# Performance work log

Hardware: AMD Instinct MI355X
Metric: run time of the kernel (lower is better)

Reference implementation:

```python
import jax, jax.numpy as jnp
import numpy as np

B, C, W, H, N = 8, 128, 48, 48, 8192


def setup_inputs() -> dict:
    key = jax.random.key(0)
    ks = jax.random.split(key, 16)
    s = 1.0 / np.sqrt(C)
    inp = {
        "feat0": jax.random.normal(ks[0], (B, C, W, H), jnp.float32),
        "feat1": jax.random.normal(ks[1], (B, C, N), jnp.float32),
        "geo_embed": jax.random.normal(ks[2], (B, W * H, C), jnp.float32),
        # Linear weights stored as [in, out]; biases [out].
        "Wq": jax.random.normal(ks[3], (C, C), jnp.float32) * s,
        "bq": jnp.zeros((C,), jnp.float32),
        "Wk": jax.random.normal(ks[4], (C, C), jnp.float32) * s,
        "bk": jnp.zeros((C,), jnp.float32),
        "Wv": jax.random.normal(ks[5], (C, C), jnp.float32) * s,
        "bv": jnp.zeros((C,), jnp.float32),
        "Wo": jax.random.normal(ks[6], (C, C), jnp.float32) * s,
        "bo": jnp.zeros((C,), jnp.float32),
        "Wg": jax.random.normal(ks[7], (C, C), jnp.float32) * s,
        "bg": jnp.zeros((C,), jnp.float32),
        "Wgate": jax.random.normal(ks[8], (2 * C, 1), jnp.float32) * (1.0 / np.sqrt(2 * C)),
        "bgate": jnp.zeros((1,), jnp.float32),
    }
    return inp


def reference(feat0, feat1, geo_embed, Wq, bq, Wk, bk, Wv, bv, Wo, bo, Wg, bg, Wgate, bgate):
    b, c, w, h = feat0.shape
    # b c w h -> b (w h) c
    q_in = feat0.reshape(b, c, w * h).transpose(0, 2, 1)
    pq = q_in @ Wq + bq  # [b, wh, c]

    geo = geo_embed @ Wg + bg  # [b, wh, c]
    gate = jax.nn.sigmoid(jnp.concatenate([pq, geo], axis=-1) @ Wgate + bgate)  # [b, wh, 1]
    pq = pq + gate * geo

    kv_in = feat1.transpose(0, 2, 1)  # [b, n, c]
    pk = kv_in @ Wk + bk
    pv = kv_in @ Wv + bv

    energy = jnp.einsum('bqc,bnc->bqn', pq, pk)  # [b, wh, n]
    # NOTE: original scales AFTER softmax (non-standard, faithful):
    attention = jax.nn.softmax(energy, axis=-1) / jnp.sqrt(jnp.asarray(c, energy.dtype))
    out = jnp.einsum('bqn,bnc->bqc', attention, pv) @ Wo + bo  # [b, wh, c]
    out = out.transpose(0, 2, 1).reshape(b, c, w, h)

    geo_r = geo.transpose(0, 2, 1).reshape(b, c, w, h)
    out = out * (1.0 + jax.nn.sigmoid(geo_r))
    out = out + feat0
    return out
```

## Files before the change

kernel.cpp:

```cpp
#include <hip/hip_runtime.h>

#define B_ 8
#define C_ 128
#define WH_ 2304
#define N_ 8192

typedef unsigned short u16;
typedef float f32x4 __attribute__((ext_vector_type(4)));
typedef short s16x8 __attribute__((ext_vector_type(8)));
typedef short s16x4 __attribute__((ext_vector_type(4)));
typedef unsigned int u32x2 __attribute__((ext_vector_type(2)));

typedef const unsigned int __attribute__((address_space(1))) ga_u32;
typedef unsigned int __attribute__((address_space(3))) lds_u32;

#define LOG2E 1.4426950408889634f
#define MOFF  64.0f

__device__ __forceinline__ float bf2f(u16 u){
    union { unsigned int i; float f; } x; x.i = ((unsigned int)u) << 16; return x.f;
}
__device__ __forceinline__ u16 f2bf(float f){
    union { float f; unsigned int i; } x; x.f = f;
    unsigned int r = x.i + 0x7fffu + ((x.i >> 16) & 1u);
    return (u16)(r >> 16);
}
__device__ __forceinline__ int swz(int row, int col){
    return row*128 + ((((col >> 3) ^ (row & 15)) << 3) | (col & 7));
}
__device__ __forceinline__ f32x4 fzero(){ f32x4 z = {0.f, 0.f, 0.f, 0.f}; return z; }
__device__ __forceinline__ f32x4 fmoff(){ f32x4 z = {-MOFF, -MOFF, -MOFF, -MOFF}; return z; }
__device__ __forceinline__ f32x4 mfma16(s16x8 a, s16x8 b, f32x4 c){
    return __builtin_amdgcn_mfma_f32_16x16x32_bf16(a, b, c, 0, 0, 0);
}
__device__ __forceinline__ void gld16(const void* g, void* l){
    __builtin_amdgcn_global_load_lds((ga_u32*)g, (lds_u32*)l, 16, 0, 0);
}
__device__ __forceinline__ s16x8 ldsf(const u16* p){ return *(const s16x8*)p; }
__device__ __forceinline__ s16x8 cvt8(const float* p){
    s16x8 r;
    #pragma unroll
    for (int j = 0; j < 8; j++) r[j] = (short)f2bf(p[j]);
    return r;
}

__global__ __launch_bounds__(256) void k_prep(
    const float* __restrict__ Wq, const float* __restrict__ Wk,
    const float* __restrict__ Wv, const float* __restrict__ Wo,
    const float* __restrict__ Wg, u16* __restrict__ Wt)
{
    const int gid = blockIdx.x*256 + threadIdx.x;
    const int mi = gid >> 14, e = gid & 16383;
    const int o = e >> 7, i = e & 127;
    const float* src = (mi==0)?Wq:(mi==1)?Wk:(mi==2)?Wv:(mi==3)?Wo:Wg;
    Wt[mi*16384 + o*128 + i] = f2bf(src[i*128 + o]);
}

__device__ __forceinline__ void proj_kv_body(
    char* smem, int blk,
    const float* __restrict__ feat1,
    const float* __restrict__ bk, const float* __restrict__ bv,
    const u16* __restrict__ Wt,
    u16* __restrict__ Kb, u16* __restrict__ Vb)
{
    u16* Af = (u16*)smem;
    const int t = threadIdx.x;
    const int b = blk >> 5;
    const int n0 = (blk & 31) * 256;
    for (int idx = t; idx < 8192; idx += 512){
        const int nl = (idx & 63) << 2, c = idx >> 6;
        const f32x4 v = *(const f32x4*)&feat1[((size_t)b*C_ + c)*N_ + n0 + nl];
        Af[swz(nl+0, c)] = f2bf(v[0]); Af[swz(nl+1, c)] = f2bf(v[1]);
        Af[swz(nl+2, c)] = f2bf(v[2]); Af[swz(nl+3, c)] = f2bf(v[3]);
    }
    __syncthreads();
    const int lane = t & 63, w = t >> 6, qq = lane >> 4, m = lane & 15;
    s16x8 aA[2][4];
    #pragma unroll
    for (int rt = 0; rt < 2; rt++){
        const int ar = w*32 + rt*16 + m;
        #pragma unroll
        for (int kt = 0; kt < 4; kt++)
            aA[rt][kt] = ldsf(&Af[ar*128 + (((kt*4 + qq) ^ (ar & 15)) << 3)]);
    }
    const u16* WkT = Wt + 16384;
    const u16* WvT = Wt + 32768;
    f32x4 acc[2][8];
    #pragma unroll
    for (int rt = 0; rt < 2; rt++){
        #pragma unroll
        for (int ct = 0; ct < 8; ct++) acc[rt][ct] = fzero();
    }
    #pragma unroll
    for (int kt = 0; kt < 4; kt++){
        #pragma unroll
        for (int ct = 0; ct < 8; ct++){
            const int bn = ct*16 + m;
            const s16x8 bf = *(const s16x8*)&WkT[bn*128 + kt*32 + qq*8];
            acc[0][ct] = mfma16(aA[0][kt], bf, acc[0][ct]);
            acc[1][ct] = mfma16(aA[1][kt], bf, acc[1][ct]);
        }
    }
    u16* Ko = (u16*)smem;
    #pragma unroll
    for (int ct = 0; ct < 8; ct++){
        const int col = ct*16 + m;
        const float bkv = bk[col];
        #pragma unroll
        for (int rt = 0; rt < 2; rt++){
            #pragma unroll
            for (int i = 0; i < 4; i++)
                Ko[swz(w*32 + rt*16 + qq*4 + i, col)] = f2bf(acc[rt][ct][i] + bkv);
        }
    }
    #pragma unroll
    for (int j = 0; j < 8; j++){
        const int chunk = j*64 + lane;
        const int row = w*32 + (chunk >> 4);
        const int cb = chunk & 15;
        s16x8 v = ldsf(&Ko[row*128 + ((cb ^ (row & 15)) << 3)]);
        *(s16x8*)&Kb[((size_t)b*N_ + n0 + row)*C_ + cb*8] = v;
    }
    #pragma unroll
    for (int rt = 0; rt < 2; rt++){
        #pragma unroll
        for (int ct = 0; ct < 8; ct++) acc[rt][ct] = fzero();
    }
    #pragma unroll
    for (int kt = 0; kt < 4; kt++){
        #pragma unroll
        for (int ct = 0; ct < 8; ct++){
            const int bn = ct*16 + m;
            const s16x8 bf = *(const s16x8*)&WvT[bn*128 + kt*32 + qq*8];
            acc[0][ct] = mfma16(aA[0][kt], bf, acc[0][ct]);
            acc[1][ct] = mfma16(aA[1][kt], bf, acc[1][ct]);
        }
    }
    __syncthreads();
    u16* Tv = (u16*)smem;
    #pragma unroll
    for (int ct = 0; ct < 8; ct++){
        const int col = ct*16 + m;
        const float bvv = bv[col];
        #pragma unroll
        for (int rt = 0; rt < 2; rt++){
            #pragma unroll
            for (int i = 0; i < 4; i++)
                Tv[col*258 + w*32 + rt*16 + qq*4 + i] = f2bf(acc[rt][ct][i] + bvv);
        }
    }
    __syncthreads();
    for (int idx = t; idx < 16384; idx += 512){
        const int c = idx >> 7, nl = (idx & 127) << 1;
        const unsigned int v = *(const unsigned int*)&Tv[c*258 + nl];
        *(unsigned int*)&Vb[((size_t)b*C_ + c)*N_ + n0 + nl] = v;
    }
}

__device__ __forceinline__ void proj_qg_body(
    char* smem, int blk,
    const float* __restrict__ feat0, const float* __restrict__ geo,
    const float* __restrict__ bq, const float* __restrict__ bg,
    const float* __restrict__ Wgate, const float* __restrict__ bgate,
    const u16* __restrict__ Wt,
    u16* __restrict__ Qb, u16* __restrict__ Gb)
{
    u16* Aq = (u16*)smem;
    const int t = threadIdx.x;
    const int b = blk / 18;
    const int r0 = (blk % 18) * 128;
    for (int idx = t; idx < 4096; idx += 512){
        const int r = (idx & 31) << 2, c = idx >> 5;
        const f32x4 v = *(const f32x4*)&feat0[((size_t)b*C_ + c)*WH_ + r0 + r];
        Aq[swz(r+0, c)] = f2bf(v[0]); Aq[swz(r+1, c)] = f2bf(v[1]);
        Aq[swz(r+2, c)] = f2bf(v[2]); Aq[swz(r+3, c)] = f2bf(v[3]);
    }
    __syncthreads();
    const int lane = t & 63, w = t >> 6, qq = lane >> 4, m = lane & 15;
    const int ar = w*16 + m;
    s16x8 aQ[4], aG[4];
    #pragma unroll
    for (int kt = 0; kt < 4; kt++){
        aQ[kt] = ldsf(&Aq[ar*128 + (((kt*4 + qq) ^ (ar & 15)) << 3)]);
        aG[kt] = cvt8(&geo[((size_t)b*WH_ + r0 + ar)*C_ + kt*32 + qq*8]);
    }
    f32x4 accq[8], accg[8];
    #pragma unroll
    for (int ct = 0; ct < 8; ct++){ accq[ct] = fzero(); accg[ct] = fzero(); }
    #pragma unroll
    for (int kt = 0; kt < 4; kt++){
        #pragma unroll
        for (int ct = 0; ct < 8; ct++){
            const int bn = ct*16 + m;
            const s16x8 b1 = *(const s16x8*)&Wt[bn*128 + kt*32 + qq*8];
            const s16x8 b2 = *(const s16x8*)&Wt[65536 + bn*128 + kt*32 + qq*8];
            accq[ct] = mfma16(aQ[kt], b1, accq[ct]);
            accg[ct] = mfma16(aG[kt], b2, accg[ct]);
        }
    }
    float bqv[8], bgv[8], w1v[8], w2v[8];
    #pragma unroll
    for (int ct = 0; ct < 8; ct++){
        int col = ct*16 + m;
        bqv[ct] = bq[col]; bgv[ct] = bg[col];
        w1v[ct] = Wgate[col]; w2v[ct] = Wgate[C_ + col];
    }
    const float bg0 = bgate[0];
    float gate[4];
    #pragma unroll
    for (int i = 0; i < 4; i++){
        float p = 0.f;
        #pragma unroll
        for (int ct = 0; ct < 8; ct++)
            p += (accq[ct][i] + bqv[ct]) * w1v[ct] + (accg[ct][i] + bgv[ct]) * w2v[ct];
        #pragma unroll
        for (int off = 1; off < 16; off <<= 1) p += __shfl_xor(p, off, 64);
        gate[i] = 1.f / (1.f + __expf(-(p + bg0)));
    }
    u16* St = Aq;
    #pragma unroll
    for (int ct = 0; ct < 8; ct++){
        #pragma unroll
        for (int i = 0; i < 4; i++){
            const float ge = accg[ct][i] + bgv[ct];
            const float pq = accq[ct][i] + bqv[ct] + gate[i] * ge;
            St[swz(w*16 + qq*4 + i, ct*16 + m)] = f2bf(pq * LOG2E);
        }
    }
    #pragma unroll
    for (int j = 0; j < 4; j++){
        const int chunk = j*64 + lane;
        const int row = w*16 + (chunk >> 4);
        const int cb = chunk & 15;
        s16x8 v = ldsf(&St[row*128 + ((cb ^ (row & 15)) << 3)]);
        *(s16x8*)&Qb[((size_t)b*WH_ + r0 + row)*C_ + cb*8] = v;
    }
    #pragma unroll
    for (int ct = 0; ct < 8; ct++){
        #pragma unroll
        for (int i = 0; i < 4; i++)
            St[swz(w*16 + qq*4 + i, ct*16 + m)] = f2bf(accg[ct][i] + bgv[ct]);
    }
    #pragma unroll
    for (int j = 0; j < 4; j++){
        const int chunk = j*64 + lane;
        const int row = w*16 + (chunk >> 4);
        const int cb = chunk & 15;
        s16x8 v = ldsf(&St[row*128 + ((cb ^ (row & 15)) << 3)]);
        *(s16x8*)&Gb[((size_t)b*WH_ + r0 + row)*C_ + cb*8] = v;
    }
}

__global__ __launch_bounds__(512, 4) void k_proj(
    const float* __restrict__ feat1,
    const float* __restrict__ bk, const float* __restrict__ bv,
    const float* __restrict__ feat0, const float* __restrict__ geo,
    const float* __restrict__ bq, const float* __restrict__ bg,
    const float* __restrict__ Wgate, const float* __restrict__ bgate,
    const u16* __restrict__ Wt,
    u16* __restrict__ Kb, u16* __restrict__ Vb,
    u16* __restrict__ Qb, u16* __restrict__ Gb)
{
    __shared__ __attribute__((aligned(16))) char smem[66048];
    if (blockIdx.x < 256)
        proj_kv_body(smem, blockIdx.x, feat1, bk, bv, Wt, Kb, Vb);
    else
        proj_qg_body(smem, blockIdx.x - 256, feat0, geo, bq, bg, Wgate, bgate, Wt, Qb, Gb);
}

__global__ __launch_bounds__(1024, 4) void k_flash(
    const u16* __restrict__ Qb, const u16* __restrict__ Kb, const u16* __restrict__ Vb,
    u16* __restrict__ Opart, float* __restrict__ Lp)
{
    __shared__ __attribute__((aligned(16))) u16 KP0[128*128];
    __shared__ __attribute__((aligned(16))) u16 KP1[128*128];
    __shared__ __attribute__((aligned(16))) u16 Vt0[128*128];
    __shared__ __attribute__((aligned(16))) u16 Vt1[128*128];
    const int t = threadIdx.x;
    const int lane = t & 63, w = t >> 6;
    const int q = lane >> 4, m = lane & 15;
    const int b = blockIdx.x & 7;
    const int s = blockIdx.x >> 3;

    f32x4 o[8];
    float lr;
    s16x8 qf[4];

    auto issue = [&](int k){
        const int u = s*18 + k;
        const int n0 = (u & 63) * 128;
        u16* KPd = (k & 1) ? KP1 : KP0;
        u16* Vtd = (k & 1) ? Vt1 : Vt0;
        #pragma unroll
        for (int j = 0; j < 2; j++){
            const int r = w*8 + j*4 + q;
            const int pr = (r & 96) | ((r & 12) << 1) | ((r & 16) >> 2) | (r & 3);
            gld16(Kb + ((size_t)b*N_ + n0 + pr)*C_ + ((m ^ (r & 15)) << 3), &KPd[(w*8 + j*4)*128]);
            gld16(Vb + ((size_t)b*C_ + r)*N_ + n0 + ((m ^ (r & 15)) << 3), &Vtd[(w*8 + j*4)*128]);
        }
    };
    auto load_q = [&](int qb){
        const size_t qrow0 = (size_t)b*WH_ + qb*256;
        #pragma unroll
        for (int kt = 0; kt < 4; kt++)
            qf[kt] = *(const s16x8*)&Qb[(qrow0 + w*16 + m)*C_ + kt*32 + q*8];
    };
    auto zero_acc = [&](){
        #pragma unroll
        for (int ct = 0; ct < 8; ct++) o[ct] = fzero();
        lr = 0.f;
    };
    auto flush = [&](int qb){
        const int sf = (qb * 64) / 18;
        const size_t pbase = ((size_t)(b*9 + qb)*5 + (s - sf)) * 256;
        #pragma unroll
        for (int ct = 0; ct < 8; ct++){
            u32x2 pk;
            pk.x = (unsigned int)f2bf(o[ct][0]) | ((unsigned int)f2bf(o[ct][1]) << 16);
            pk.y = (unsigned int)f2bf(o[ct][2]) | ((unsigned int)f2bf(o[ct][3]) << 16);
            *(u32x2*)&Opart[(pbase + w*16 + m)*128 + ct*16 + q*4] = pk;
        }
        float l0 = lr;
        l0 += __shfl_xor(l0, 16, 64); l0 += __shfl_xor(l0, 32, 64);
        if (q == 0) Lp[pbase + w*16 + m] = l0;
    };

    issue(0);
    int cur_qb = (s*18) >> 6;
    load_q(cur_qb);
    zero_acc();

    for (int k = 0; k < 18; k++){
        __syncthreads();
        if (k < 17) issue(k + 1);
        const u16* KPc = (k & 1) ? KP1 : KP0;
        const u16* Vtc = (k & 1) ? Vt1 : Vt0;

        #pragma unroll
        for (int h = 0; h < 2; h++){
            s16x4 pexp[4];
            #pragma unroll
            for (int n2 = 0; n2 < 4; n2++){
                const int nt = h*4 + n2;
                f32x4 s0 = fmoff();
                const int bn = nt*16 + m;
                #pragma unroll
                for (int kt = 0; kt < 4; kt++){
                    s16x8 kf = ldsf(&KPc[bn*128 + (((kt*4 + q) ^ (bn & 15)) << 3)]);
                    s0 = mfma16(kf, qf[kt], s0);
                }
                #pragma unroll
                for (int i = 0; i < 4; i++){
                    float e0 = exp2f(s0[i]);
                    lr += e0;
                    pexp[n2][i] = (short)f2bf(e0);
                }
            }
            const s16x8 p80 = __builtin_shufflevector(pexp[0], pexp[1], 0,1,2,3,4,5,6,7);
            const s16x8 p81 = __builtin_shufflevector(pexp[2], pexp[3], 0,1,2,3,4,5,6,7);
            #pragma unroll
            for (int ct = 0; ct < 8; ct++){
                const int cc = ct*16 + m;
                const int pair0 = h*2;
                s16x8 vf0 = ldsf(&Vtc[cc*128 + ((((pair0+0)*4 + q) ^ (cc & 15)) << 3)]);
                s16x8 vf1 = ldsf(&Vtc[cc*128 + ((((pair0+1)*4 + q) ^ (cc & 15)) << 3)]);
                o[ct] = mfma16(vf0, p80, o[ct]);
                o[ct] = mfma16(vf1, p81, o[ct]);
            }
        }
        const int nqb = (k < 17) ? ((s*18 + k + 1) >> 6) : -1;
        if (nqb != cur_qb){
            flush(cur_qb);
            if (nqb >= 0){ load_q(nqb); zero_acc(); cur_qb = nqb; }
        }
    }
}

__global__ __launch_bounds__(256) void k_out(
    const u16* __restrict__ Opart, const float* __restrict__ Lp,
    const float* __restrict__ bo, const u16* __restrict__ Wt,
    const u16* __restrict__ Gb, const float* __restrict__ feat0,
    float* __restrict__ outp)
{
    __shared__ __attribute__((aligned(16))) u16 AO[128*128];
    __shared__ u16 Tr[128*130];
    const int t = threadIdx.x;
    const int bqt = blockIdx.x;
    const int qt2 = bqt >> 1, half = bqt & 1;
    const int b = qt2 / 9, qb = qt2 % 9;
    const int gr0 = qb*256 + half*128;
    const u16* WoT = Wt + 49152;
    const float rsC = 0.088388347648318447f;
    const int sf = (qb*64) / 18;
    const int sl = (qb*64 + 63) / 18;
    const int cnt = sl - sf + 1;
    for (int idx = t; idx < 128*16; idx += 256){
        int r = idx >> 4, cb = idx & 15;
        float num[8];
        #pragma unroll
        for (int j = 0; j < 8; j++) num[j] = 0.f;
        float den = 0.f;
        for (int ss = 0; ss < cnt; ss++){
            const size_t base = ((size_t)qt2*5 + ss)*256 + half*128 + r;
            s16x8 v = *(const s16x8*)&Opart[base*128 + cb*8];
            #pragma unroll
            for (int j = 0; j < 8; j++) num[j] += bf2f((u16)v[j]);
            den += Lp[base];
        }
        const float sc = rsC / den;
        s16x8 o8;
        #pragma unroll
        for (int j = 0; j < 8; j++) o8[j] = (short)f2bf(num[j] * sc);
        *(s16x8*)&AO[r*128 + ((cb ^ (r & 15)) << 3)] = o8;
    }
    __syncthreads();
    const int lane = t & 63, w = t >> 6;
    const int q = lane >> 4, m = lane & 15;
    const int rw = w * 32;
    f32x4 acc[2][8];
    #pragma unroll
    for (int rt = 0; rt < 2; rt++){
        #pragma unroll
        for (int ct = 0; ct < 8; ct++) acc[rt][ct] = fzero();
    }
    #pragma unroll
    for (int kt = 0; kt < 4; kt++){
        s16x8 a0, a1;
        { const int ar = rw + m;      a0 = ldsf(&AO[ar*128 + (((kt*4 + q) ^ (ar & 15)) << 3)]); }
        { const int ar = rw + 16 + m; a1 = ldsf(&AO[ar*128 + (((kt*4 + q) ^ (ar & 15)) << 3)]); }
        #pragma unroll
        for (int ct = 0; ct < 8; ct++){
            const s16x8 bb = *(const s16x8*)&WoT[(ct*16 + m)*128 + kt*32 + q*8];
            acc[0][ct] = mfma16(a0, bb, acc[0][ct]);
            acc[1][ct] = mfma16(a1, bb, acc[1][ct]);
        }
    }
    #pragma unroll
    for (int ct = 0; ct < 8; ct++){
        const int col = ct*16 + m;
        const float bov = bo[col];
        #pragma unroll
        for (int rt = 0; rt < 2; rt++){
            #pragma unroll
            for (int i = 0; i < 4; i++){
                const int rl = rw + rt*16 + q*4 + i;
                const float gv = bf2f(Gb[((size_t)b*WH_ + gr0 + rl)*C_ + col]);
                const float sg = 1.f / (1.f + __expf(-gv));
                Tr[rl*130 + col] = f2bf((acc[rt][ct][i] + bov) * (1.f + sg));
            }
        }
    }
    __syncthreads();
    for (int idx = t; idx < 128*128; idx += 256){
        int c = idx >> 7, wh = idx & 127;
        float v = bf2f(Tr[wh*130 + c]) + feat0[(size_t)(b*C_ + c)*WH_ + gr0 + wh];
        outp[(size_t)(b*C_ + c)*WH_ + gr0 + wh] = v;
    }
}

extern "C" void kernel_launch(void* const* d_in, const int* in_sizes, int n_in,
                              void* d_out, int out_size, void* d_ws, size_t ws_size,
                              hipStream_t stream)
{
    (void)in_sizes; (void)n_in; (void)out_size; (void)ws_size;
    const float* feat0 = (const float*)d_in[0];
    const float* feat1 = (const float*)d_in[1];
    const float* geo   = (const float*)d_in[2];
    const float* Wq = (const float*)d_in[3];  const float* bq = (const float*)d_in[4];
    const float* Wk = (const float*)d_in[5];  const float* bk = (const float*)d_in[6];
    const float* Wv = (const float*)d_in[7];  const float* bv = (const float*)d_in[8];
    const float* Wo = (const float*)d_in[9];  const float* bo = (const float*)d_in[10];
    const float* Wg = (const float*)d_in[11]; const float* bg = (const float*)d_in[12];
    const float* Wgate = (const float*)d_in[13]; const float* bgate = (const float*)d_in[14];
    float* outp = (float*)d_out;
    char* ws = (char*)d_ws;
    size_t off = 0;
    auto alloc = [&](size_t bytes) -> void* {
        void* p = (void*)(ws + off);
        off += (bytes + 255) & ~(size_t)255;
        return p;
    };
    u16* Qb = (u16*)alloc((size_t)B_*WH_*C_*2);
    u16* Gb = (u16*)alloc((size_t)B_*WH_*C_*2);
    u16* Kb = (u16*)alloc((size_t)B_*N_*C_*2);
    u16* Vb = (u16*)alloc((size_t)B_*N_*C_*2);
    u16* Opart = (u16*)alloc((size_t)72*5*256*128*2);
    float* Lp  = (float*)alloc((size_t)72*5*256*4);
    u16* Wt = (u16*)alloc((size_t)5*16384*2);

    k_prep <<<dim3(320), dim3(256), 0, stream>>>(Wq, Wk, Wv, Wo, Wg, Wt);
    k_proj <<<dim3(400), dim3(512), 0, stream>>>(feat1, bk, bv, feat0, geo, bq, bg,
                                                 Wgate, bgate, Wt, Kb, Vb, Qb, Gb);
    k_flash<<<dim3(256), dim3(1024), 0, stream>>>(Qb, Kb, Vb, Opart, Lp);
    k_out  <<<dim3(144), dim3(256), 0, stream>>>(Opart, Lp, bo, Wt, Gb, feat0, outp);
}
```

Measured before the change: 303.4 us.

## Split projection kernel, use packed bf16 converts and MFMA row-sum in flash loop

The merged projection kernel is split into separate K/V and Q/G kernels with smaller tiles and more blocks. The K/V kernel writes V directly from registers instead of staging it through LDS. The flash attention loop now converts exponentials with the hardware packed bf16 instruction and computes the softmax denominator with an MFMA against a ones vector, which removes scalar adds and cross-lane shuffles. This adds one kernel launch, and the row sum is now taken over bf16-rounded probabilities, which is consistent with what feeds the PV MFMA.

Result: faster. 286.1 us (-5.7%).

```diff
diff --git a/kernel.cpp b/kernel.cpp
--- a/kernel.cpp
+++ b/kernel.cpp
@@ -25,6 +25,11 @@
     unsigned int r = x.i + 0x7fffu + ((x.i >> 16) & 1u);
     return (u16)(r >> 16);
 }
+__device__ __forceinline__ unsigned int cvtpk(float a, float b){
+    unsigned int r;
+    asm("v_cvt_pk_bf16_f32 %0, %1, %2" : "=v"(r) : "v"(a), "v"(b));
+    return r;
+}
 __device__ __forceinline__ int swz(int row, int col){
     return row*128 + ((((col >> 3) ^ (row & 15)) << 3) | (col & 7));
 }
@@ -56,121 +61,93 @@
     Wt[mi*16384 + o*128 + i] = f2bf(src[i*128 + o]);
 }
 
-__device__ __forceinline__ void proj_kv_body(
-    char* smem, int blk,
+__global__ __launch_bounds__(512, 4) void k_proj_kv(
     const float* __restrict__ feat1,
     const float* __restrict__ bk, const float* __restrict__ bv,
     const u16* __restrict__ Wt,
     u16* __restrict__ Kb, u16* __restrict__ Vb)
 {
-    u16* Af = (u16*)smem;
+    __shared__ __attribute__((aligned(16))) u16 Af[128*128];
     const int t = threadIdx.x;
-    const int b = blk >> 5;
-    const int n0 = (blk & 31) * 256;
-    for (int idx = t; idx < 8192; idx += 512){
-        const int nl = (idx & 63) << 2, c = idx >> 6;
+    const int b = blockIdx.x >> 6;
+    const int n0 = (blockIdx.x & 63) * 128;
+    for (int idx = t; idx < 128*32; idx += 512){
+        const int nl = (idx & 31) << 2, c = idx >> 5;
         const f32x4 v = *(const f32x4*)&feat1[((size_t)b*C_ + c)*N_ + n0 + nl];
         Af[swz(nl+0, c)] = f2bf(v[0]); Af[swz(nl+1, c)] = f2bf(v[1]);
         Af[swz(nl+2, c)] = f2bf(v[2]); Af[swz(nl+3, c)] = f2bf(v[3]);
     }
     __syncthreads();
     const int lane = t & 63, w = t >> 6, qq = lane >> 4, m = lane & 15;
-    s16x8 aA[2][4];
-    #pragma unroll
-    for (int rt = 0; rt < 2; rt++){
-        const int ar = w*32 + rt*16 + m;
-        #pragma unroll
-        for (int kt = 0; kt < 4; kt++)
-            aA[rt][kt] = ldsf(&Af[ar*128 + (((kt*4 + qq) ^ (ar & 15)) << 3)]);
-    }
+    const int ar = w*16 + m;
+    s16x8 aA[4];
+    #pragma unroll
+    for (int kt = 0; kt < 4; kt++)
+        aA[kt] = ldsf(&Af[ar*128 + (((kt*4 + qq) ^ (ar & 15)) << 3)]);
     const u16* WkT = Wt + 16384;
     const u16* WvT = Wt + 32768;
-    f32x4 acc[2][8];
-    #pragma unroll
-    for (int rt = 0; rt < 2; rt++){
-        #pragma unroll
-        for (int ct = 0; ct < 8; ct++) acc[rt][ct] = fzero();
-    }
+    f32x4 acc[8];
+    #pragma unroll
+    for (int ct = 0; ct < 8; ct++) acc[ct] = fzero();
     #pragma unroll
     for (int kt = 0; kt < 4; kt++){
         #pragma unroll
         for (int ct = 0; ct < 8; ct++){
-            const int bn = ct*16 + m;
-            const s16x8 bf = *(const s16x8*)&WkT[bn*128 + kt*32 + qq*8];
-            acc[0][ct] = mfma16(aA[0][kt], bf, acc[0][ct]);
-            acc[1][ct] = mfma16(aA[1][kt], bf, acc[1][ct]);
-        }
-    }
-    u16* Ko = (u16*)smem;
+            const s16x8 bf = *(const s16x8*)&WkT[(ct*16 + m)*128 + kt*32 + qq*8];
+            acc[ct] = mfma16(aA[kt], bf, acc[ct]);
+        }
+    }
+    u16* Ko = Af;
     #pragma unroll
     for (int ct = 0; ct < 8; ct++){
         const int col = ct*16 + m;
         const float bkv = bk[col];
         #pragma unroll
-        for (int rt = 0; rt < 2; rt++){
-            #pragma unroll
-            for (int i = 0; i < 4; i++)
-                Ko[swz(w*32 + rt*16 + qq*4 + i, col)] = f2bf(acc[rt][ct][i] + bkv);
-        }
-    }
-    #pragma unroll
-    for (int j = 0; j < 8; j++){
+        for (int i = 0; i < 4; i++)
+            Ko[swz(w*16 + qq*4 + i, col)] = f2bf(acc[ct][i] + bkv);
+    }
+    #pragma unroll
+    for (int j = 0; j < 4; j++){
         const int chunk = j*64 + lane;
-        const int row = w*32 + (chunk >> 4);
+        const int row = w*16 + (chunk >> 4);
         const int cb = chunk & 15;
         s16x8 v = ldsf(&Ko[row*128 + ((cb ^ (row & 15)) << 3)]);
         *(s16x8*)&Kb[((size_t)b*N_ + n0 + row)*C_ + cb*8] = v;
     }
     #pragma unroll
-    for (int rt = 0; rt < 2; rt++){
-        #pragma unroll
-        for (int ct = 0; ct < 8; ct++) acc[rt][ct] = fzero();
-    }
+    for (int ct = 0; ct < 8; ct++) acc[ct] = fzero();
     #pragma unroll
     for (int kt = 0; kt < 4; kt++){
         #pragma unroll
         for (int ct = 0; ct < 8; ct++){
-            const int bn = ct*16 + m;
-            const s16x8 bf = *(const s16x8*)&WvT[bn*128 + kt*32 + qq*8];
-            acc[0][ct] = mfma16(aA[0][kt], bf, acc[0][ct]);
-            acc[1][ct] = mfma16(aA[1][kt], bf, acc[1][ct]);
-        }
-    }
-    __syncthreads();
-    u16* Tv = (u16*)smem;
+            const s16x8 bf = *(const s16x8*)&WvT[(ct*16 + m)*128 + kt*32 + qq*8];
+            acc[ct] = mfma16(aA[kt], bf, acc[ct]);
+        }
+    }
     #pragma unroll
     for (int ct = 0; ct < 8; ct++){
         const int col = ct*16 + m;
         const float bvv = bv[col];
-        #pragma unroll
-        for (int rt = 0; rt < 2; rt++){
-            #pragma unroll
-            for (int i = 0; i < 4; i++)
-                Tv[col*258 + w*32 + rt*16 + qq*4 + i] = f2bf(acc[rt][ct][i] + bvv);
-        }
-    }
-    __syncthreads();
-    for (int idx = t; idx < 16384; idx += 512){
-        const int c = idx >> 7, nl = (idx & 127) << 1;
-        const unsigned int v = *(const unsigned int*)&Tv[c*258 + nl];
-        *(unsigned int*)&Vb[((size_t)b*C_ + c)*N_ + n0 + nl] = v;
-    }
-}
-
-__device__ __forceinline__ void proj_qg_body(
-    char* smem, int blk,
+        u32x2 pk;
+        pk.x = cvtpk(acc[ct][0] + bvv, acc[ct][1] + bvv);
+        pk.y = cvtpk(acc[ct][2] + bvv, acc[ct][3] + bvv);
+        *(u32x2*)&Vb[((size_t)b*C_ + col)*N_ + n0 + w*16 + qq*4] = pk;
+    }
+}
+
+__global__ __launch_bounds__(256, 3) void k_proj_qg(
     const float* __restrict__ feat0, const float* __restrict__ geo,
     const float* __restrict__ bq, const float* __restrict__ bg,
     const float* __restrict__ Wgate, const float* __restrict__ bgate,
     const u16* __restrict__ Wt,
     u16* __restrict__ Qb, u16* __restrict__ Gb)
 {
-    u16* Aq = (u16*)smem;
+    __shared__ __attribute__((aligned(16))) u16 Aq[64*128];
     const int t = threadIdx.x;
-    const int b = blk / 18;
-    const int r0 = (blk % 18) * 128;
-    for (int idx = t; idx < 4096; idx += 512){
-        const int r = (idx & 31) << 2, c = idx >> 5;
+    const int b = blockIdx.x / 36;
+    const int r0 = (blockIdx.x % 36) * 64;
+    for (int idx = t; idx < 64*32; idx += 256){
+        const int r = (idx & 15) << 2, c = idx >> 4;
         const f32x4 v = *(const f32x4*)&feat0[((size_t)b*C_ + c)*WH_ + r0 + r];
         Aq[swz(r+0, c)] = f2bf(v[0]); Aq[swz(r+1, c)] = f2bf(v[1]);
         Aq[swz(r+2, c)] = f2bf(v[2]); Aq[swz(r+3, c)] = f2bf(v[3]);
@@ -198,11 +175,17 @@
             accg[ct] = mfma16(aG[kt], b2, accg[ct]);
         }
     }
-    float bqv[8], bgv[8], w1v[8], w2v[8];
-    #pragma unroll
-    for (int ct = 0; ct < 8; ct++){
-        int col = ct*16 + m;
-        bqv[ct] = bq[col]; bgv[ct] = bg[col];
+    #pragma unroll
+    for (int ct = 0; ct < 8; ct++){
+        const int col = ct*16 + m;
+        const float bqv = bq[col], bgv = bg[col];
+        #pragma unroll
+        for (int i = 0; i < 4; i++){ accq[ct][i] += bqv; accg[ct][i] += bgv; }
+    }
+    float w1v[8], w2v[8];
+    #pragma unroll
+    for (int ct = 0; ct < 8; ct++){
+        const int col = ct*16 + m;
         w1v[ct] = Wgate[col]; w2v[ct] = Wgate[C_ + col];
     }
     const float bg0 = bgate[0];
@@ -212,7 +195,7 @@
         float p = 0.f;
         #pragma unroll
         for (int ct = 0; ct < 8; ct++)
-            p += (accq[ct][i] + bqv[ct]) * w1v[ct] + (accg[ct][i] + bgv[ct]) * w2v[ct];
+            p += accq[ct][i] * w1v[ct] + accg[ct][i] * w2v[ct];
         #pragma unroll
         for (int off = 1; off < 16; off <<= 1) p += __shfl_xor(p, off, 64);
         gate[i] = 1.f / (1.f + __expf(-(p + bg0)));
@@ -222,8 +205,7 @@
     for (int ct = 0; ct < 8; ct++){
         #pragma unroll
         for (int i = 0; i < 4; i++){
-            const float ge = accg[ct][i] + bgv[ct];
-            const float pq = accq[ct][i] + bqv[ct] + gate[i] * ge;
+            const float pq = accq[ct][i] + gate[i] * accg[ct][i];
             St[swz(w*16 + qq*4 + i, ct*16 + m)] = f2bf(pq * LOG2E);
         }
     }
@@ -239,7 +221,7 @@
     for (int ct = 0; ct < 8; ct++){
         #pragma unroll
         for (int i = 0; i < 4; i++)
-            St[swz(w*16 + qq*4 + i, ct*16 + m)] = f2bf(accg[ct][i] + bgv[ct]);
+            St[swz(w*16 + qq*4 + i, ct*16 + m)] = f2bf(accg[ct][i]);
     }
     #pragma unroll
     for (int j = 0; j < 4; j++){
@@ -249,23 +231,6 @@
         s16x8 v = ldsf(&St[row*128 + ((cb ^ (row & 15)) << 3)]);
         *(s16x8*)&Gb[((size_t)b*WH_ + r0 + row)*C_ + cb*8] = v;
     }
-}
-
-__global__ __launch_bounds__(512, 4) void k_proj(
-    const float* __restrict__ feat1,
-    const float* __restrict__ bk, const float* __restrict__ bv,
-    const float* __restrict__ feat0, const float* __restrict__ geo,
-    const float* __restrict__ bq, const float* __restrict__ bg,
-    const float* __restrict__ Wgate, const float* __restrict__ bgate,
-    const u16* __restrict__ Wt,
-    u16* __restrict__ Kb, u16* __restrict__ Vb,
-    u16* __restrict__ Qb, u16* __restrict__ Gb)
-{
-    __shared__ __attribute__((aligned(16))) char smem[66048];
-    if (blockIdx.x < 256)
-        proj_kv_body(smem, blockIdx.x, feat1, bk, bv, Wt, Kb, Vb);
-    else
-        proj_qg_body(smem, blockIdx.x - 256, feat0, geo, bq, bg, Wgate, bgate, Wt, Qb, Gb);
 }
 
 __global__ __launch_bounds__(1024, 4) void k_flash(
@@ -283,8 +248,11 @@
     const int s = blockIdx.x >> 3;
 
     f32x4 o[8];
-    float lr;
+    f32x4 l_acc;
     s16x8 qf[4];
+    s16x8 ones8;
+    #pragma unroll
+    for (int j = 0; j < 8; j++) ones8[j] = (short)0x3F80;
 
     auto issue = [&](int k){
         const int u = s*18 + k;
@@ -308,7 +276,7 @@
     auto zero_acc = [&](){
         #pragma unroll
         for (int ct = 0; ct < 8; ct++) o[ct] = fzero();
-        lr = 0.f;
+        l_acc = fzero();
     };
     auto flush = [&](int qb){
         const int sf = (qb * 64) / 18;
@@ -316,13 +284,11 @@
         #pragma unroll
         for (int ct = 0; ct < 8; ct++){
             u32x2 pk;
-            pk.x = (unsigned int)f2bf(o[ct][0]) | ((unsigned int)f2bf(o[ct][1]) << 16);
-            pk.y = (unsigned int)f2bf(o[ct][2]) | ((unsigned int)f2bf(o[ct][3]) << 16);
+            pk.x = cvtpk(o[ct][0], o[ct][1]);
+            pk.y = cvtpk(o[ct][2], o[ct][3]);
             *(u32x2*)&Opart[(pbase + w*16 + m)*128 + ct*16 + q*4] = pk;
         }
-        float l0 = lr;
-        l0 += __shfl_xor(l0, 16, 64); l0 += __shfl_xor(l0, 32, 64);
-        if (q == 0) Lp[pbase + w*16 + m] = l0;
+        if (q == 0) Lp[pbase + w*16 + m] = l_acc[0];
     };
 
     issue(0);
@@ -349,15 +315,15 @@
                     s16x8 kf = ldsf(&KPc[bn*128 + (((kt*4 + q) ^ (bn & 15)) << 3)]);
                     s0 = mfma16(kf, qf[kt], s0);
                 }
-                #pragma unroll
-                for (int i = 0; i < 4; i++){
-                    float e0 = exp2f(s0[i]);
-                    lr += e0;
-                    pexp[n2][i] = (short)f2bf(e0);
-                }
+                union { u32x2 u; s16x4 v; } pp;
+                pp.u.x = cvtpk(exp2f(s0[0]), exp2f(s0[1]));
+                pp.u.y = cvtpk(exp2f(s0[2]), exp2f(s0[3]));
+                pexp[n2] = pp.v;
             }
             const s16x8 p80 = __builtin_shufflevector(pexp[0], pexp[1], 0,1,2,3,4,5,6,7);
             const s16x8 p81 = __builtin_shufflevector(pexp[2], pexp[3], 0,1,2,3,4,5,6,7);
+            l_acc = mfma16(ones8, p80, l_acc);
+            l_acc = mfma16(ones8, p81, l_acc);
             #pragma unroll
             for (int ct = 0; ct < 8; ct++){
                 const int cc = ct*16 + m;
@@ -488,9 +454,9 @@
     float* Lp  = (float*)alloc((size_t)72*5*256*4);
     u16* Wt = (u16*)alloc((size_t)5*16384*2);
 
-    k_prep <<<dim3(320), dim3(256), 0, stream>>>(Wq, Wk, Wv, Wo, Wg, Wt);
-    k_proj <<<dim3(400), dim3(512), 0, stream>>>(feat1, bk, bv, feat0, geo, bq, bg,
-                                                 Wgate, bgate, Wt, Kb, Vb, Qb, Gb);
-    k_flash<<<dim3(256), dim3(1024), 0, stream>>>(Qb, Kb, Vb, Opart, Lp);
-    k_out  <<<dim3(144), dim3(256), 0, stream>>>(Opart, Lp, bo, Wt, Gb, feat0, outp);
-}
+    k_prep   <<<dim3(320), dim3(256), 0, stream>>>(Wq, Wk, Wv, Wo, Wg, Wt);
+    k_proj_kv<<<dim3(512), dim3(512), 0, stream>>>(feat1, bk, bv, Wt, Kb, Vb);
+    k_proj_qg<<<dim3(288), dim3(256), 0, stream>>>(feat0, geo, bq, bg, Wgate, bgate, Wt, Qb, Gb);
+    k_flash  <<<dim3(256), dim3(1024), 0, stream>>>(Qb, Kb, Vb, Opart, Lp);
+    k_out    <<<dim3(144), dim3(256), 0, stream>>>(Opart, Lp, bo, Wt, Gb, feat0, outp);
+}
```
